# Optimization experiments

Measured on AMD Instinct MI355X. Metric: run time of the kernel, lower is better.

The kernel has to match this reference:

```python
import jax, jax.numpy as jnp
import numpy as np

PROJ = 8192     # projDim
THRESH = 1e-8   # numerical-stability epsilon for signed sqrt
L2_EPS = 1e-12  # eps of torch F.normalize


def setup_inputs() -> dict:
    key = jax.random.key(0)
    k1, k2, k3, k4, k5 = jax.random.split(key, 5)
    B, C, H, W = 16, 512, 14, 14
    x = jax.random.normal(k1, (B, C, H, W), dtype=jnp.float32)
    h1 = jax.random.randint(k2, (C,), 0, PROJ, dtype=jnp.int32)
    h2 = jax.random.randint(k3, (C,), 0, PROJ, dtype=jnp.int32)
    s1 = (2 * jax.random.randint(k4, (C,), 0, 2) - 1).astype(jnp.float32)
    s2 = (2 * jax.random.randint(k5, (C,), 0, 2) - 1).astype(jnp.float32)
    return {"x": x, "s1": s1, "s2": s2, "h1": h1, "h2": h2}


def reference(x, s1, s2, h1, h2):
    # x: [B, C, H, W]; h*: [C] hash buckets in [0, PROJ); s*: [C] signs (+-1)
    B, C, H, W = x.shape
    x_flat = jnp.transpose(x, (0, 2, 3, 1)).reshape(-1, C)  # [N, C], N = B*H*W

    def count_sketch(s, h):
        # Equivalent to x_flat @ M with M[c, h[c]] = s[c]: scatter-add of
        # sign-weighted channels into PROJ bins.  -> [N, PROJ]
        return jax.ops.segment_sum((x_flat * s).T, h, num_segments=PROJ).T

    fft1 = jnp.fft.fft(count_sketch(s1, h1), axis=-1)
    fft2 = jnp.fft.fft(count_sketch(s2, h2), axis=-1)
    conv = jnp.fft.ifft(fft1 * fft2, axis=-1).real       # [N, PROJ]
    y = conv.reshape(B, H, W, PROJ).sum(axis=(1, 2))      # sum pool -> [B, PROJ]
    y = jnp.sign(y) * jnp.sqrt(jnp.abs(y) + THRESH)       # signed sqrt
    norm = jnp.linalg.norm(y, axis=1, keepdims=True)
    return y / jnp.maximum(norm, L2_EPS)                  # l2 normalize (dim=1)
```

## Files before the change

### kernel.cpp

```cpp
#include <hip/hip_runtime.h>
#include <math.h>

#define PROJ 8192
#define NB   16
#define NC   512
#define HW   196
#define NKC  7
#define LST  40

typedef __attribute__((ext_vector_type(8))) short bf16x8;
typedef __attribute__((ext_vector_type(4))) short short4v;
typedef __attribute__((ext_vector_type(4))) float f32x4;

__device__ __forceinline__ unsigned bf16_rne(float f) {
    unsigned u = __builtin_bit_cast(unsigned, f);
    return (u + 0x7fffu + ((u >> 16) & 1u)) >> 16;
}

__global__ __launch_bounds__(512, 2)
void cbp_gram_mfma(const float* __restrict__ x,
                   const float* __restrict__ s1,
                   const float* __restrict__ s2,
                   const int*   __restrict__ h1,
                   const int*   __restrict__ h2,
                   float* __restrict__ ws) {
    __shared__ float sk[PROJ];
    __shared__ short Ah[128 * LST];
    __shared__ short Al[128 * LST];
    __shared__ short Bh[128 * LST];
    __shared__ short Bl[128 * LST];
    __shared__ int   lh1[128], lh2[128];
    __shared__ float lsA[128], lsB[128];

    const int tid = threadIdx.x;
    const int blk = blockIdx.x;
    const int b    = 2 * (blk & 7) + (blk >> 7);
    const int tile = (blk >> 3) & 15;
    const int I = tile >> 2, J = tile & 3;
    const int c1base = I * 128;
    const int c2base = J * 128;

    const int lane = tid & 63;
    const int wave = tid >> 6;
    const int quad = lane >> 4;
    const int l15  = lane & 15;
    const int wr   = (wave >> 1) * 32;
    const int wc   = (wave & 1) * 64;

    for (int i = tid; i < PROJ; i += 512) sk[i] = 0.f;
    if (tid < 128) {
        lh1[tid] = h1[c1base + tid];  lsA[tid] = s1[c1base + tid];
        lh2[tid] = h2[c2base + tid];  lsB[tid] = s2[c2base + tid];
    }

    const float* xa = x + ((size_t)b * NC + c1base) * HW;
    const float* xb = x + ((size_t)b * NC + c2base) * HW;

    f32x4 acc[2][4];
#pragma unroll
    for (int i = 0; i < 2; ++i)
#pragma unroll
        for (int j = 0; j < 4; ++j) acc[i][j] = (f32x4){0.f, 0.f, 0.f, 0.f};

    const int sr0 = tid >> 3;
    const int sq  = tid & 7;

    float4 pa[2], pb[2];
    {
        const int kk = 4 * sq;
        const bool ok = (kk + 3 < HW);
#pragma unroll
        for (int h = 0; h < 2; ++h) {
            const int r = sr0 + 64 * h;
            pa[h] = ok ? *(const float4*)&xa[r * HW + kk] : (float4){0.f,0.f,0.f,0.f};
            pb[h] = ok ? *(const float4*)&xb[r * HW + kk] : (float4){0.f,0.f,0.f,0.f};
        }
    }

    for (int kc = 0; kc < NKC; ++kc) {
        __syncthreads();
#pragma unroll
        for (int h = 0; h < 2; ++h) {
            const int r = sr0 + 64 * h;
            const float sA = lsA[r], sB = lsB[r];
            const float fa[4] = {pa[h].x*sA, pa[h].y*sA, pa[h].z*sA, pa[h].w*sA};
            const float fb[4] = {pb[h].x*sB, pb[h].y*sB, pb[h].z*sB, pb[h].w*sB};
            short4v ah, al, bh, bl;
#pragma unroll
            for (int c = 0; c < 4; ++c) {
                const unsigned ha_ = bf16_rne(fa[c]);
                ah[c] = (short)ha_;
                al[c] = (short)bf16_rne(fa[c] - __builtin_bit_cast(float, ha_ << 16));
                const unsigned hb_ = bf16_rne(fb[c]);
                bh[c] = (short)hb_;
                bl[c] = (short)bf16_rne(fb[c] - __builtin_bit_cast(float, hb_ << 16));
            }
            *(short4v*)&Ah[r * LST + 4 * sq] = ah;
            *(short4v*)&Al[r * LST + 4 * sq] = al;
            *(short4v*)&Bh[r * LST + 4 * sq] = bh;
            *(short4v*)&Bl[r * LST + 4 * sq] = bl;
        }
        if (kc + 1 < NKC) {
            const int kk = (kc + 1) * 32 + 4 * sq;
            const bool ok = (kk + 3 < HW);
#pragma unroll
            for (int h = 0; h < 2; ++h) {
                const int r = sr0 + 64 * h;
                pa[h] = ok ? *(const float4*)&xa[r * HW + kk] : (float4){0.f,0.f,0.f,0.f};
                pb[h] = ok ? *(const float4*)&xb[r * HW + kk] : (float4){0.f,0.f,0.f,0.f};
            }
        }
        __syncthreads();

        bf16x8 ahf[2], alf[2], bhf[4], blf[4];
#pragma unroll
        for (int i = 0; i < 2; ++i) {
            const int ra = wr + i * 16 + l15;
            ahf[i] = *(const bf16x8*)&Ah[ra * LST + quad * 8];
            alf[i] = *(const bf16x8*)&Al[ra * LST + quad * 8];
        }
#pragma unroll
        for (int j = 0; j < 4; ++j) {
            const int rb = wc + j * 16 + l15;
            bhf[j] = *(const bf16x8*)&Bh[rb * LST + quad * 8];
            blf[j] = *(const bf16x8*)&Bl[rb * LST + quad * 8];
        }
#pragma unroll
        for (int i = 0; i < 2; ++i)
#pragma unroll
            for (int j = 0; j < 4; ++j) {
                acc[i][j] = __builtin_amdgcn_mfma_f32_16x16x32_bf16(ahf[i], bhf[j], acc[i][j], 0, 0, 0);
                acc[i][j] = __builtin_amdgcn_mfma_f32_16x16x32_bf16(ahf[i], blf[j], acc[i][j], 0, 0, 0);
                acc[i][j] = __builtin_amdgcn_mfma_f32_16x16x32_bf16(alf[i], bhf[j], acc[i][j], 0, 0, 0);
            }
    }
    __syncthreads();

#pragma unroll
    for (int i = 0; i < 2; ++i) {
        const int lr0 = wr + i * 16 + quad * 4;
#pragma unroll
        for (int j = 0; j < 4; ++j) {
            const int h2v = lh2[wc + j * 16 + l15];
#pragma unroll
            for (int rg = 0; rg < 4; ++rg) {
                const int bin = (lh1[lr0 + rg] + h2v) & (PROJ - 1);
                atomicAdd(&sk[bin], acc[i][j][rg]);
            }
        }
    }
    __syncthreads();

    float4* dst = (float4*)(ws + (size_t)blk * PROJ);
    const float4* src = (const float4*)sk;
    for (int i = tid; i < PROJ / 4; i += 512) dst[i] = src[i];
}

__global__ __launch_bounds__(256)
void cbp_reduce(const float* __restrict__ ws, float* __restrict__ y,
                float* __restrict__ ssqp) {
    const int blk = blockIdx.x;
    const int b   = blk >> 5;
    const int seg = blk & 31;
    const int tid = threadIdx.x;
    const int bin = seg * 256 + tid;

    const int pbase = ((b & 1) << 7) | (b >> 1);
    float s = 0.f;
#pragma unroll
    for (int t = 0; t < 16; ++t)
        s += ws[(size_t)(pbase | (t << 3)) * PROJ + bin];

    const float m = sqrtf(fabsf(s) + 1e-8f);
    const float o = (s > 0.f) ? m : (s < 0.f ? -m : 0.f);
    y[b * PROJ + bin] = o;

    __shared__ float red[256];
    red[tid] = o * o;
    __syncthreads();
#pragma unroll
    for (int st = 128; st >= 1; st >>= 1) {
        if (tid < st) red[tid] += red[tid + st];
        __syncthreads();
    }
    if (tid == 0) ssqp[blk] = red[0];
}

__global__ __launch_bounds__(256)
void cbp_normalize(float* __restrict__ y, const float* __restrict__ ssqp) {
    const int b   = blockIdx.x >> 1;
    const int off = (blockIdx.x & 1) * 4096;
    const int tid = threadIdx.x;
    float ssq = 0.f;
#pragma unroll
    for (int i = 0; i < 32; ++i) ssq += ssqp[b * 32 + i];
    const float inv = 1.0f / fmaxf(sqrtf(ssq), 1e-12f);

    float4* row = (float4*)&y[(size_t)b * PROJ + off];
#pragma unroll
    for (int j = 0; j < 4; ++j) {
        float4 v = row[j * 256 + tid];
        v.x *= inv; v.y *= inv; v.z *= inv; v.w *= inv;
        row[j * 256 + tid] = v;
    }
}

extern "C" void kernel_launch(void* const* d_in, const int* in_sizes, int n_in,
                              void* d_out, int out_size, void* d_ws, size_t ws_size,
                              hipStream_t stream) {
    const float* x  = (const float*)d_in[0];
    const float* s1 = (const float*)d_in[1];
    const float* s2 = (const float*)d_in[2];
    const int*   h1 = (const int*)d_in[3];
    const int*   h2 = (const int*)d_in[4];
    float* y    = (float*)d_out;
    float* ws   = (float*)d_ws;
    float* ssqp = ws + (size_t)256 * PROJ;

    hipLaunchKernelGGL(cbp_gram_mfma, dim3(256), dim3(512), 0, stream,
                       x, s1, s2, h1, h2, ws);
    hipLaunchKernelGGL(cbp_reduce, dim3(512), dim3(256), 0, stream, ws, y, ssqp);
    hipLaunchKernelGGL(cbp_normalize, dim3(32), dim3(256), 0, stream, y, ssqp);
}
```

Before: 103.8 us.

## Accumulate per-batch sketches with global atomics and fuse reduce/normalize kernels

Each gram block now atomically adds its shared-memory sketch into a per-batch global buffer instead of writing a private partial, and the buffer is zeroed with a memset. The separate reduce and normalize kernels are replaced by one finalize kernel per batch that applies the signed sqrt, reduces the sum of squares with wave shuffles and writes the normalized output. This removes a 8 MB partial-sum write and read-back and one kernel launch. In exchange it adds a memset launch, 16-way atomic contention per bin, and a finalize grid of only 16 blocks.

```diff
diff --git a/kernel.cpp b/kernel.cpp
--- a/kernel.cpp
+++ b/kernel.cpp
@@ -23,7 +23,7 @@
                    const float* __restrict__ s2,
                    const int*   __restrict__ h1,
                    const int*   __restrict__ h2,
-                   float* __restrict__ ws) {
+                   float* __restrict__ gsk) {
     __shared__ float sk[PROJ];
     __shared__ short Ah[128 * LST];
     __shared__ short Al[128 * LST];
@@ -151,57 +151,49 @@
     }
     __syncthreads();
 
-    float4* dst = (float4*)(ws + (size_t)blk * PROJ);
-    const float4* src = (const float4*)sk;
-    for (int i = tid; i < PROJ / 4; i += 512) dst[i] = src[i];
-}
-
-__global__ __launch_bounds__(256)
-void cbp_reduce(const float* __restrict__ ws, float* __restrict__ y,
-                float* __restrict__ ssqp) {
-    const int blk = blockIdx.x;
-    const int b   = blk >> 5;
-    const int seg = blk & 31;
+    float* gs = gsk + (size_t)b * PROJ;
+    for (int i = tid; i < PROJ; i += 512) atomicAdd(&gs[i], sk[i]);
+}
+
+__device__ __forceinline__ float ssqrt(float s) {
+    const float m = sqrtf(fabsf(s) + 1e-8f);
+    return (s > 0.f) ? m : (s < 0.f ? -m : 0.f);
+}
+
+__global__ __launch_bounds__(512)
+void cbp_finalize(const float* __restrict__ gsk, float* __restrict__ y) {
+    __shared__ float red[8];
+    const int b   = blockIdx.x;
     const int tid = threadIdx.x;
-    const int bin = seg * 256 + tid;
-
-    const int pbase = ((b & 1) << 7) | (b >> 1);
-    float s = 0.f;
-#pragma unroll
-    for (int t = 0; t < 16; ++t)
-        s += ws[(size_t)(pbase | (t << 3)) * PROJ + bin];
-
-    const float m = sqrtf(fabsf(s) + 1e-8f);
-    const float o = (s > 0.f) ? m : (s < 0.f ? -m : 0.f);
-    y[b * PROJ + bin] = o;
-
-    __shared__ float red[256];
-    red[tid] = o * o;
+    const float4* gp = (const float4*)(gsk + (size_t)b * PROJ);
+
+    float4 ov[4];
+    float ssq = 0.f;
+#pragma unroll
+    for (int g = 0; g < 4; ++g) {
+        const float4 s = gp[tid + 512 * g];
+        float4 o;
+        o.x = ssqrt(s.x); o.y = ssqrt(s.y); o.z = ssqrt(s.z); o.w = ssqrt(s.w);
+        ov[g] = o;
+        ssq += o.x * o.x + o.y * o.y + o.z * o.z + o.w * o.w;
+    }
+
+    float v = ssq;
+#pragma unroll
+    for (int off = 32; off >= 1; off >>= 1) v += __shfl_xor(v, off, 64);
+    if ((tid & 63) == 0) red[tid >> 6] = v;
     __syncthreads();
-#pragma unroll
-    for (int st = 128; st >= 1; st >>= 1) {
-        if (tid < st) red[tid] += red[tid + st];
-        __syncthreads();
-    }
-    if (tid == 0) ssqp[blk] = red[0];
-}
-
-__global__ __launch_bounds__(256)
-void cbp_normalize(float* __restrict__ y, const float* __restrict__ ssqp) {
-    const int b   = blockIdx.x >> 1;
-    const int off = (blockIdx.x & 1) * 4096;
-    const int tid = threadIdx.x;
-    float ssq = 0.f;
-#pragma unroll
-    for (int i = 0; i < 32; ++i) ssq += ssqp[b * 32 + i];
-    const float inv = 1.0f / fmaxf(sqrtf(ssq), 1e-12f);
-
-    float4* row = (float4*)&y[(size_t)b * PROJ + off];
-#pragma unroll
-    for (int j = 0; j < 4; ++j) {
-        float4 v = row[j * 256 + tid];
-        v.x *= inv; v.y *= inv; v.z *= inv; v.w *= inv;
-        row[j * 256 + tid] = v;
+    float tot = 0.f;
+#pragma unroll
+    for (int w = 0; w < 8; ++w) tot += red[w];
+    const float inv = 1.0f / fmaxf(sqrtf(tot), 1e-12f);
+
+    float4* yp = (float4*)(y + (size_t)b * PROJ);
+#pragma unroll
+    for (int g = 0; g < 4; ++g) {
+        float4 o = ov[g];
+        o.x *= inv; o.y *= inv; o.z *= inv; o.w *= inv;
+        yp[tid + 512 * g] = o;
     }
 }
 
@@ -213,12 +205,11 @@
     const float* s2 = (const float*)d_in[2];
     const int*   h1 = (const int*)d_in[3];
     const int*   h2 = (const int*)d_in[4];
-    float* y    = (float*)d_out;
-    float* ws   = (float*)d_ws;
-    float* ssqp = ws + (size_t)256 * PROJ;
-
+    float* y   = (float*)d_out;
+    float* gsk = (float*)d_ws;
+
+    hipMemsetAsync(gsk, 0, (size_t)NB * PROJ * sizeof(float), stream);
     hipLaunchKernelGGL(cbp_gram_mfma, dim3(256), dim3(512), 0, stream,
-                       x, s1, s2, h1, h2, ws);
-    hipLaunchKernelGGL(cbp_reduce, dim3(512), dim3(256), 0, stream, ws, y, ssqp);
-    hipLaunchKernelGGL(cbp_normalize, dim3(32), dim3(256), 0, stream, y, ssqp);
-}
+                       x, s1, s2, h1, h2, gsk);
+    hipLaunchKernelGGL(cbp_finalize, dim3(16), dim3(512), 0, stream, gsk, y);
+}
```

After: 109.6 us. 1.06x slower.
